# Kernel tuning notes

Hardware: AMD Instinct MI355X
Metric: run time of the kernel (lower is better)

## Reference

```python
import jax, jax.numpy as jnp
import numpy as np

B, N_INP, N_HID = 524288, 32, 256
NE, NI = 200, 56                      # excitatory / inhibitory columns, NE+NI == N_HID
W_E, W_I = 0.5, 0.5
WIN_E, WIN_I = 1.0, 1.0
RHO = 0.9                             # target spectral radius of h2h
DT, RC, BIAS = 0.01, 1.0, 0.0
THRESHOLD, RESET = 1.0, 0.0
LEAKY_BETA, LEAKY_THRESH = 0.9, 1.0   # snn.Leaky(beta=0.9) defaults


def setup_inputs() -> dict:
    key = jax.random.key(0)
    kx, kx2h, ke, ki = jax.random.split(key, 4)
    x = jax.random.normal(kx, (B, N_INP), dtype=jnp.float32)

    # x2h: uniform(0,1) scaled columnwise by [win_e]*Ne ++ [win_i]*Ni
    col_scale = jnp.concatenate([jnp.full((NE,), WIN_E), jnp.full((NI,), WIN_I)]).astype(jnp.float32)
    x2h = jax.random.uniform(kx2h, (N_INP, N_HID), dtype=jnp.float32) * col_scale

    # h2h: [w_e*U(0,1) | -w_i*U(0,1)] then rescaled to spectral radius RHO
    h2h_e = W_E * jax.random.uniform(ke, (N_HID, NE), dtype=jnp.float32)
    h2h_i = -W_I * jax.random.uniform(ki, (N_HID, NI), dtype=jnp.float32)
    h2h = jnp.concatenate([h2h_e, h2h_i], axis=1)
    eig_max = np.max(np.abs(np.linalg.eigvals(np.asarray(h2h, dtype=np.float64))))
    h2h = (h2h * (RHO / eig_max)).astype(jnp.float32)

    return {"x": x, "x2h": x2h, "h2h": h2h}


def reference(x, x2h, h2h):
    # forward() unsqueezes a length-1 time axis, so the LIF loop runs exactly once
    # with zero-initialized states. NOTE arg swap in the original call:
    # LIFcell(x, hy, u) called as LIFcell(x_t, u_state, hy_state):
    #   - spike/threshold/reset acts on hy_state (zeros)
    #   - recurrent matmul uses u_state (zeros)
    u_state = jnp.zeros((x.shape[0], h2h.shape[0]), dtype=x.dtype)   # [B, n_hid]
    hy_state = jnp.zeros_like(u_state)

    spk = (hy_state > THRESHOLD).astype(x.dtype)
    hy_state = jnp.where(spk == 1.0, RESET, hy_state)

    u_dot = -hy_state + (u_state @ h2h + x @ x2h + BIAS)             # [B, n_hid]
    u = hy_state + u_dot * (RC * DT)

    # hy = snn.Leaky(u)[0] is computed in the original but appended to hy_list,
    # which is never returned, so it does not affect the outputs.
    return (u, spk)
```

## Files before the change

### kernel.cpp

```cpp
#include <hip/hip_runtime.h>
#include <stdint.h>


#define NHID 256
#define NINP 32
#define RPC  8

typedef float __attribute__((ext_vector_type(4))) f32x4;
typedef float __attribute__((ext_vector_type(2))) f32x2;

__device__ __forceinline__ void stage_chunk(const float* src_lane, void* lds_wave_base) {
    __builtin_amdgcn_global_load_lds(
        (const __attribute__((address_space(1))) uint32_t*)src_lane,
        (__attribute__((address_space(3))) uint32_t*)lds_wave_base,
        16, 0, 0);
}

__global__ __launch_bounds__(256, 4) void lsm_kernel(
    const float* __restrict__ x, const float* __restrict__ x2h,
    float* __restrict__ u, float* __restrict__ spk,
    int B, int nwaves)
{
    __shared__ float xbuf[4][2][RPC * NINP];

    const int lane = threadIdx.x & 63;
    const int wv   = threadIdx.x >> 6;
    const int wid  = __builtin_amdgcn_readfirstlane(blockIdx.x * 4 + wv);

    const int half = wid & 1;
    const int c    = half * 128 + lane * 2;

    f32x2 w[NINP];
#pragma unroll
    for (int k = 0; k < NINP; ++k) {
        f32x2 t = *reinterpret_cast<const f32x2*>(x2h + k * NHID + c);
        w[k] = t * 0.01f;
    }

    const int cw  = wid >> 1;
    const int ncw = nwaves >> 1;
    const int total_chunks = B / RPC;
    const int nch = (total_chunks - cw + ncw - 1) / ncw;
    if (nch <= 0) return;

    const float* src0 = x + (size_t)cw * (RPC * NINP) + lane * 4;
    const size_t src_stride = (size_t)ncw * (RPC * NINP);

    stage_chunk(src0, &xbuf[wv][0][0]);
    if (nch > 1) stage_chunk(src0 + src_stride, &xbuf[wv][1][0]);

    for (int i = 0; i < nch; ++i) {
        if (i == 0) {
            if (nch > 1) asm volatile("s_waitcnt vmcnt(1)" ::: "memory");
            else         asm volatile("s_waitcnt vmcnt(0)" ::: "memory");
        } else if (i == nch - 1) {
            asm volatile("s_waitcnt vmcnt(16)" ::: "memory");
        } else {
            asm volatile("s_waitcnt vmcnt(17)" ::: "memory");
        }

        const float* xb = &xbuf[wv][i & 1][0];
        const size_t row0 = ((size_t)cw + (size_t)i * ncw) * RPC;

#pragma unroll 2
        for (int r = 0; r < RPC; ++r) {
            const f32x4* xr = (const f32x4*)(xb + r * NINP);
            f32x2 acc = {0.f, 0.f};
#pragma unroll
            for (int g = 0; g < 8; ++g) {
                f32x4 xq = xr[g];
                acc += w[4 * g + 0] * xq.x;
                acc += w[4 * g + 1] * xq.y;
                acc += w[4 * g + 2] * xq.z;
                acc += w[4 * g + 3] * xq.w;
            }
            const size_t base = (row0 + r) * NHID + c;
            __builtin_nontemporal_store(acc, (f32x2*)(u + base));
            f32x2 z = {0.f, 0.f};
            __builtin_nontemporal_store(z, (f32x2*)(spk + base));
        }

        if (i + 2 < nch) stage_chunk(src0 + (size_t)(i + 2) * src_stride, &xbuf[wv][i & 1][0]);
    }
}

extern "C" void kernel_launch(void* const* d_in, const int* in_sizes, int n_in,
                              void* d_out, int out_size, void* d_ws, size_t ws_size,
                              hipStream_t stream) {
    const float* x   = (const float*)d_in[0];
    const float* x2h = (const float*)d_in[1];

    const int B = in_sizes[0] / NINP;
    float* u   = (float*)d_out;
    float* spk = u + (size_t)B * NHID;

    const int threads = 256;
    const int blocks  = 4096;
    const int nwaves  = blocks * (threads / 64);
    lsm_kernel<<<blocks, threads, 0, stream>>>(x, x2h, u, spk, B, nwaves);
}
```

Baseline: 204.8 us.

## Split blocks into compute blocks and dedicated zero-fill blocks for spk

Workgroups are now split by role: 9 of every 16 compute u from x and x2h, and the remaining 7 only write zeros to the spk output using 16-byte nontemporal stores. The compute path drops its per-row spk stores, so the vmcnt wait counts shrink from 17/16 to 9/8. The aim is to overlap a pure zero-fill write stream with the compute stream and to use wider stores for spk. In exchange, fewer waves do the matmul, so each compute wave handles more chunks, and the split ratio is hard-coded.

After: 233.0 us. 1.14x slower.

```diff
diff --git a/kernel.cpp b/kernel.cpp
--- a/kernel.cpp
+++ b/kernel.cpp
@@ -5,6 +5,12 @@
 #define NHID 256
 #define NINP 32
 #define RPC  8
+
+#define BLOCKS_TOTAL 4096
+#define COMP_PER16   9
+#define FILL_PER16   (16 - COMP_PER16)
+#define NCOMP_BLOCKS (BLOCKS_TOTAL / 16 * COMP_PER16)
+#define NFILL_BLOCKS (BLOCKS_TOTAL / 16 * FILL_PER16)
 
 typedef float __attribute__((ext_vector_type(4))) f32x4;
 typedef float __attribute__((ext_vector_type(2))) f32x2;
@@ -18,17 +24,29 @@
 
 __global__ __launch_bounds__(256, 4) void lsm_kernel(
     const float* __restrict__ x, const float* __restrict__ x2h,
-    float* __restrict__ u, float* __restrict__ spk,
-    int B, int nwaves)
+    float* __restrict__ u, float* __restrict__ spk, int B)
 {
     __shared__ float xbuf[4][2][RPC * NINP];
 
+    const int b16 = blockIdx.x & 15;
+
+    if (b16 >= COMP_PER16) {
+        const int fb = (blockIdx.x >> 4) * FILL_PER16 + (b16 - COMP_PER16);
+        const size_t nf4 = (size_t)B * NHID / 4;
+        const size_t stride = (size_t)NFILL_BLOCKS * 256;
+        f32x4* spk4 = (f32x4*)spk;
+        f32x4 z = {0.f, 0.f, 0.f, 0.f};
+        for (size_t j = (size_t)fb * 256 + threadIdx.x; j < nf4; j += stride)
+            __builtin_nontemporal_store(z, spk4 + j);
+        return;
+    }
+
+    const int cb   = (blockIdx.x >> 4) * COMP_PER16 + b16;
     const int lane = threadIdx.x & 63;
     const int wv   = threadIdx.x >> 6;
-    const int wid  = __builtin_amdgcn_readfirstlane(blockIdx.x * 4 + wv);
+    const int wid  = __builtin_amdgcn_readfirstlane(cb * 4 + wv);
 
-    const int half = wid & 1;
-    const int c    = half * 128 + lane * 2;
+    const int c = (wid & 1) * 128 + lane * 2;
 
     f32x2 w[NINP];
 #pragma unroll
@@ -38,7 +56,7 @@
     }
 
     const int cw  = wid >> 1;
-    const int ncw = nwaves >> 1;
+    const int ncw = NCOMP_BLOCKS * 4 / 2;
     const int total_chunks = B / RPC;
     const int nch = (total_chunks - cw + ncw - 1) / ncw;
     if (nch <= 0) return;
@@ -54,9 +72,9 @@
             if (nch > 1) asm volatile("s_waitcnt vmcnt(1)" ::: "memory");
             else         asm volatile("s_waitcnt vmcnt(0)" ::: "memory");
         } else if (i == nch - 1) {
-            asm volatile("s_waitcnt vmcnt(16)" ::: "memory");
+            asm volatile("s_waitcnt vmcnt(8)" ::: "memory");
         } else {
-            asm volatile("s_waitcnt vmcnt(17)" ::: "memory");
+            asm volatile("s_waitcnt vmcnt(9)" ::: "memory");
         }
 
         const float* xb = &xbuf[wv][i & 1][0];
@@ -74,10 +92,7 @@
                 acc += w[4 * g + 2] * xq.z;
                 acc += w[4 * g + 3] * xq.w;
             }
-            const size_t base = (row0 + r) * NHID + c;
-            __builtin_nontemporal_store(acc, (f32x2*)(u + base));
-            f32x2 z = {0.f, 0.f};
-            __builtin_nontemporal_store(z, (f32x2*)(spk + base));
+            __builtin_nontemporal_store(acc, (f32x2*)(u + (row0 + r) * NHID + c));
         }
 
         if (i + 2 < nch) stage_chunk(src0 + (size_t)(i + 2) * src_stride, &xbuf[wv][i & 1][0]);
@@ -94,8 +109,5 @@
     float* u   = (float*)d_out;
     float* spk = u + (size_t)B * NHID;
 
-    const int threads = 256;
-    const int blocks  = 4096;
-    const int nwaves  = blocks * (threads / 64);
-    lsm_kernel<<<blocks, threads, 0, stream>>>(x, x2h, u, spk, B, nwaves);
+    lsm_kernel<<<BLOCKS_TOTAL, 256, 0, stream>>>(x, x2h, u, spk, B);
 }
```
